# Kernel tuning notes

Hardware: AMD Instinct MI355X
Metric: run time of the kernel (lower is better)

## Reference

```python
import jax, jax.numpy as jnp
import numpy as np

S, B, IN = 8, 8192, 2      # obs seq_len, batch, input_size
E, H, OUT, PRED = 256, 1024, 2, 12  # embed, rnn_size, output_size, pred_len


def setup_inputs() -> dict:
    key = jax.random.key(0)
    ks = jax.random.split(key, 20)
    w = lambda k, shape, fan: (jax.random.normal(k, shape, jnp.float32) / np.sqrt(fan))
    return {
        "obs_traj": jax.random.normal(ks[0], (S, B, IN), jnp.float32),
        # input embedding Linear(IN -> E)
        "W_emb": w(ks[1], (E, IN), IN), "b_emb": jnp.zeros((E,), jnp.float32),
        # LSTM layer 0: input E -> H  (torch gate order i,f,g,o)
        "W_ih0": w(ks[2], (4 * H, E), E), "W_hh0": w(ks[3], (4 * H, H), H),
        "b_ih0": jnp.zeros((4 * H,), jnp.float32), "b_hh0": jnp.zeros((4 * H,), jnp.float32),
        # LSTM layer 1: input H -> H
        "W_ih1": w(ks[4], (4 * H, H), H), "W_hh1": w(ks[5], (4 * H, H), H),
        "b_ih1": jnp.zeros((4 * H,), jnp.float32), "b_hh1": jnp.zeros((4 * H,), jnp.float32),
        # output_seq MLP: H -> 32 -> 16 -> OUT
        "W1": w(ks[6], (32, H), H), "b1": jnp.zeros((32,), jnp.float32),
        "W2": w(ks[7], (16, 32), 32), "b2": jnp.zeros((16,), jnp.float32),
        "W3": w(ks[8], (OUT, 16), 16), "b3": jnp.zeros((OUT,), jnp.float32),
    }


def reference(obs_traj, W_emb, b_emb, W_ih0, W_hh0, b_ih0, b_hh0,
              W_ih1, W_hh1, b_ih1, b_hh1, W1, b1, W2, b2, W3, b3):
    # Dropout layers are identity in eval mode.
    def embed(x):
        return jax.nn.relu(x @ W_emb.T + b_emb)

    def cell(x, h, c, Wih, Whh, bih, bhh):
        g = x @ Wih.T + h @ Whh.T + (bih + bhh)          # [B, 4H]
        i, f, gg, o = jnp.split(g, 4, axis=-1)
        c = jax.nn.sigmoid(f) * c + jax.nn.sigmoid(i) * jnp.tanh(gg)
        h = jax.nn.sigmoid(o) * jnp.tanh(c)
        return h, c

    def lstm_step(hc, x):
        h0, c0, h1, c1 = hc
        h0, c0 = cell(x, h0, c0, W_ih0, W_hh0, b_ih0, b_hh0)
        h1, c1 = cell(h0, h1, c1, W_ih1, W_hh1, b_ih1, b_hh1)
        return (h0, c0, h1, c1), h1

    def mlp(h):
        h = jax.nn.relu(h @ W1.T + b1)
        h = jax.nn.relu(h @ W2.T + b2)
        return h @ W3.T + b3

    z = jnp.zeros((B, H), obs_traj.dtype)
    hc = (z, z, z, z)

    # --- encoding: run LSTM over the observed trajectory ---
    emb_obs = embed(obs_traj)                             # [S, B, E]
    hc, _ = jax.lax.scan(lambda c, x: lstm_step(c, x), hc, emb_obs)

    curr = obs_traj[-1]                                   # [B, IN]
    curr_emb = embed(curr)

    def dec_step(carry, _):
        hc, curr, curr_emb = carry
        hc, out = lstm_step(hc, curr_emb)                 # out: [B, H]
        nxt = curr + mlp(out)                             # displacement decode
        return (hc, nxt, embed(nxt)), nxt

    _, preds = jax.lax.scan(dec_step, (hc, curr, curr_emb), None, length=PRED)
    return preds                                          # [PRED, B, OUT]
```

## Files before the change

kernel.cpp:

```cpp
#include <hip/hip_runtime.h>
#include <hip/hip_bf16.h>
#include <stdint.h>

typedef __hip_bfloat16 bf16;
typedef __attribute__((ext_vector_type(8))) short bf16x8;
typedef __attribute__((ext_vector_type(4))) float f32x4;
typedef __attribute__((ext_vector_type(8))) unsigned short us8;

#define NB 8192
#define NE 256
#define NH 1024

__device__ __forceinline__ float bf2f(unsigned short u) {
  union { unsigned int i; float f; } x; x.i = ((unsigned int)u) << 16; return x.f;
}
__device__ __forceinline__ float sigm(float x) {
  return __builtin_amdgcn_rcpf(1.f + __expf(-x));
}
__device__ __forceinline__ float tanh_f(float x) {
  return 1.f - 2.f * __builtin_amdgcn_rcpf(1.f + __expf(2.f * x));
}

#define BAR() __builtin_amdgcn_s_barrier()
#define FENCE() asm volatile("" ::: "memory")
#define LGKME() asm volatile("s_waitcnt lgkmcnt(0)" ::: "memory")
#define VMW(N) asm volatile("s_waitcnt vmcnt(" #N ")" ::: "memory")

#define GLDS(G, S)                                                            \
  __builtin_amdgcn_global_load_lds(                                           \
      (const __attribute__((address_space(1))) void*)(G),                     \
      (__attribute__((address_space(3))) void*)(S), 16, 0, 0)

#define MFMA32(MH)                                                            \
  do {                                                                        \
    _Pragma("unroll") for (int i_ = 0; i_ < 4; ++i_)                          \
      _Pragma("unroll") for (int g_ = 0; g_ < 4; ++g_) {                      \
        acc[(MH)*4 + i_][g_] = __builtin_amdgcn_mfma_f32_16x16x32_bf16(       \
            af[i_], bv[g_], acc[(MH)*4 + i_][g_], 0, 0, 0);                   \
        acc[(MH)*4 + i_][g_] = __builtin_amdgcn_mfma_f32_16x16x32_bf16(       \
            af[4 + i_], bv[4 + g_], acc[(MH)*4 + i_][g_], 0, 0, 0);           \
      }                                                                       \
  } while (0)

#define LDA8(BUF, MH)                                                         \
  do {                                                                        \
    const char* Ab_ = (const char*)&As[BUF][0][0];                            \
    _Pragma("unroll") for (int i_ = 0; i_ < 4; ++i_) {                        \
      int ro_ = (wr * 128 + (MH)*64 + i_ * 16 + l15) * 128;                   \
      af[i_]     = *(const bf16x8*)(Ab_ + ro_ + co0);                         \
      af[4 + i_] = *(const bf16x8*)(Ab_ + ro_ + co1);                         \
    }                                                                         \
  } while (0)

#define LDB8(BUF)                                                             \
  do {                                                                        \
    const char* Bb_ = (const char*)&Bs[BUF][0][0];                            \
    _Pragma("unroll") for (int g_ = 0; g_ < 4; ++g_) {                        \
      int ro_ = (g_ * 64 + nc * 16 + l15) * 128;                              \
      bv[g_]     = *(const bf16x8*)(Bb_ + ro_ + co0);                         \
      bv[4 + g_] = *(const bf16x8*)(Bb_ + ro_ + co1);                         \
    }                                                                         \
  } while (0)

struct CellP {
  const bf16* X; const bf16* Hin;
  const bf16* Wih; const bf16* Whh;
  const float* bias; float* Cst; bf16* Hout;
  int ldx, Kx, Kh, czero;
};

__global__ __launch_bounds__(512, 2) void k_cell(CellP PA, CellP PB, int nA)
{
  __shared__ bf16 As[2][256][64];
  __shared__ bf16 Bs[2][256][64];

  const CellP p = (blockIdx.x < (unsigned)nA) ? PA : PB;
  const int bid = (blockIdx.x < (unsigned)nA) ? blockIdx.x : (blockIdx.x - nA);

  const int tid = threadIdx.x;
  const int l = tid & 63;
  const int l15 = l & 15;
  const int wv = tid >> 6;
  const int wr = wv >> 2;
  const int nc = wv & 3;

  const int xcd = bid & 7, j = bid >> 3;
  const int m0 = (xcd * 4 + (j & 3)) * 256;
  const int hc0 = (j >> 2) * 64;

  const int NT = (p.Kx + p.Kh) >> 6;
  const int T = NT >> 1;

  const int rowid = tid >> 3;
  const int ch = (tid & 7) ^ (rowid & 7);
  const int ch8 = ch * 8;
  const int wv8 = wv * 8;

  const int co0 = (((l >> 4) + 0) ^ (l & 7)) * 16;
  const int co1 = (((l >> 4) + 4) ^ (l & 7)) * 16;

  f32x4 acc[8][4];
  f32x4 zero4 = {0.f, 0.f, 0.f, 0.f};
#pragma unroll
  for (int i = 0; i < 8; ++i)
#pragma unroll
    for (int j2 = 0; j2 < 4; ++j2) acc[i][j2] = zero4;

  auto stage_a = [&](int buf, int half, int kt) {
    int kc = kt << 6;
    const bf16* src; int ldi;
    if (kc < p.Kx) { src = p.X + kc; ldi = p.ldx; }
    else           { src = p.Hin + (kc - p.Kx); ldi = NH; }
#pragma unroll
    for (int rnd = 0; rnd < 2; ++rnd) {
      int tr = rnd * 128 + half * 64;
      const bf16* gp = src + (unsigned)((m0 + tr + rowid) * ldi + ch8);
      GLDS(gp, &As[buf][tr + wv8][0]);
    }
  };
  auto stage_b = [&](int buf, int half, int kt) {
    int kc = kt << 6;
    const bf16* src; int ldi;
    if (kc < p.Kx) { src = p.Wih + kc; ldi = p.Kx; }
    else           { src = p.Whh + (kc - p.Kx); ldi = NH; }
#pragma unroll
    for (int rnd = 0; rnd < 2; ++rnd) {
      int gate = rnd * 2 + half;
      const bf16* gp = src + (unsigned)((gate * NH + hc0 + rowid) * ldi + ch8);
      GLDS(gp, &Bs[buf][gate * 64 + wv8][0]);
    }
  };

  stage_a(0, 0, 0);
  stage_a(0, 1, 0);
  stage_b(0, 0, 0);
  stage_b(0, 1, 0);
  stage_a(1, 0, 1);
  VMW(2);
  BAR();

  for (int t = 0; t < T; ++t) {
    const int kt1 = 2 * t + 1;
    const bool last = (t == T - 1);
    bf16x8 af[8], bv[8];

    LDB8(0); LDA8(0, 0);
    stage_a(1, 1, kt1);
    stage_b(1, 0, kt1);
    stage_b(1, 1, kt1);
    FENCE(); BAR();
    MFMA32(0);
    LGKME();
    BAR();

    LDA8(0, 1);
    if (!last) stage_a(0, 0, kt1 + 1);
    FENCE(); BAR();
    MFMA32(1);
    LGKME();
    if (last) { VMW(0); } else { VMW(2); }
    BAR();

    LDB8(1); LDA8(1, 0);
    if (!last) {
      stage_a(0, 1, kt1 + 1);
      stage_b(0, 0, kt1 + 1);
      stage_b(0, 1, kt1 + 1);
    }
    FENCE(); BAR();
    MFMA32(0);
    LGKME();
    BAR();

    LDA8(1, 1);
    if (!last) stage_a(1, 0, kt1 + 2);
    FENCE(); BAR();
    MFMA32(1);
    LGKME();
    if (!last) { VMW(2); }
    BAR();
  }

  const int ecol = hc0 + nc * 16 + l15;
  const float bi = p.bias[ecol];
  const float bff = p.bias[NH + ecol];
  const float bg = p.bias[2 * NH + ecol];
  const float bo = p.bias[3 * NH + ecol];
  const int r0 = m0 + wr * 128 + ((l >> 4) << 2);
#pragma unroll
  for (int m = 0; m < 8; ++m) {
#pragma unroll
    for (int r = 0; r < 4; ++r) {
      int row = r0 + m * 16 + r;
      unsigned idx = (unsigned)(row * NH) + ecol;
      float gi = sigm(acc[m][0][r] + bi);
      float gf = sigm(acc[m][1][r] + bff);
      float gg = tanh_f(acc[m][2][r] + bg);
      float go = sigm(acc[m][3][r] + bo);
      float cold = p.czero ? 0.f : p.Cst[idx];
      float cn = gf * cold + gi * gg;
      p.Cst[idx] = cn;
      p.Hout[idx] = __float2bfloat16(go * tanh_f(cn));
    }
  }
}

__global__ __launch_bounds__(256) void k_mlp(
    const bf16* __restrict__ h1, const bf16* __restrict__ W1b, const float* __restrict__ b1,
    const float* __restrict__ W2, const float* __restrict__ b2,
    const float* __restrict__ W3, const float* __restrict__ b3,
    const float* __restrict__ cin, float* __restrict__ cout,
    float* __restrict__ preds, const float* __restrict__ Wemb,
    const float* __restrict__ bemb, bf16* __restrict__ embout)
{
  const int l = threadIdx.x & 63;
  const int row = blockIdx.x * 4 + (threadIdx.x >> 6);

  const us8* hp = (const us8*)(h1 + (size_t)row * NH + l * 16);
  us8 hv0 = hp[0], hv1 = hp[1];
  float h[16];
#pragma unroll
  for (int j = 0; j < 8; ++j) { h[j] = bf2f(hv0[j]); h[8 + j] = bf2f(hv1[j]); }

  float y1[32];
#pragma unroll
  for (int j = 0; j < 32; ++j) {
    const us8* wp = (const us8*)(W1b + (size_t)j * NH + l * 16);
    us8 w0 = wp[0], w1 = wp[1];
    float d = 0.f;
#pragma unroll
    for (int k = 0; k < 8; ++k) {
      d = fmaf(h[k], bf2f(w0[k]), d);
      d = fmaf(h[8 + k], bf2f(w1[k]), d);
    }
#pragma unroll
    for (int off2 = 32; off2 > 0; off2 >>= 1) d += __shfl_xor(d, off2);
    y1[j] = fmaxf(d + b1[j], 0.f);
  }

  float y2[16];
#pragma unroll
  for (int m = 0; m < 16; ++m) {
    float s = b2[m];
#pragma unroll
    for (int j = 0; j < 32; ++j) s = fmaf(W2[m * 32 + j], y1[j], s);
    y2[m] = fmaxf(s, 0.f);
  }
  float o0 = b3[0], o1 = b3[1];
#pragma unroll
  for (int k = 0; k < 16; ++k) {
    o0 = fmaf(W3[k], y2[k], o0);
    o1 = fmaf(W3[16 + k], y2[k], o1);
  }
  float n0 = cin[row * 2] + o0;
  float n1 = cin[row * 2 + 1] + o1;
  if (l == 0) {
    preds[row * 2] = n0; preds[row * 2 + 1] = n1;
    cout[row * 2] = n0;  cout[row * 2 + 1] = n1;
  }
#pragma unroll
  for (int q = 0; q < 4; ++q) {
    int e = l + q * 64;
    float v = fmaf(n0, Wemb[e * 2], fmaf(n1, Wemb[e * 2 + 1], bemb[e]));
    embout[(size_t)row * NE + e] = __float2bfloat16(fmaxf(v, 0.f));
  }
}

__global__ void k_embed(const float* __restrict__ x, const float* __restrict__ W,
                        const float* __restrict__ b, bf16* __restrict__ out) {
  const int l = threadIdx.x & 63;
  const int row = (blockIdx.x * 256 + threadIdx.x) >> 6;
  float x0 = x[row * 2], x1 = x[row * 2 + 1];
#pragma unroll
  for (int q = 0; q < 4; ++q) {
    int e = l + q * 64;
    float v = fmaf(x0, W[e * 2], fmaf(x1, W[e * 2 + 1], b[e]));
    out[(size_t)row * NE + e] = __float2bfloat16(fmaxf(v, 0.f));
  }
}

__global__ void k_f2b(const float* __restrict__ in, bf16* __restrict__ out, int n) {
  int i = (blockIdx.x * 256 + threadIdx.x) * 4;
  if (i >= n) return;
  float4 v = *(const float4*)(in + i);
  out[i] = __float2bfloat16(v.x);
  out[i + 1] = __float2bfloat16(v.y);
  out[i + 2] = __float2bfloat16(v.z);
  out[i + 3] = __float2bfloat16(v.w);
}

__global__ void k_badd(const float* __restrict__ a, const float* __restrict__ b,
                       float* __restrict__ o, int n) {
  int i = blockIdx.x * 256 + threadIdx.x;
  if (i < n) o[i] = a[i] + b[i];
}

extern "C" void kernel_launch(void* const* d_in, const int* in_sizes, int n_in,
                              void* d_out, int out_size, void* d_ws, size_t ws_size,
                              hipStream_t stream) {
  const float* obs   = (const float*)d_in[0];
  const float* Wemb  = (const float*)d_in[1];
  const float* bemb  = (const float*)d_in[2];
  const float* Wih0f = (const float*)d_in[3];
  const float* Whh0f = (const float*)d_in[4];
  const float* bih0  = (const float*)d_in[5];
  const float* bhh0  = (const float*)d_in[6];
  const float* Wih1f = (const float*)d_in[7];
  const float* Whh1f = (const float*)d_in[8];
  const float* bih1  = (const float*)d_in[9];
  const float* bhh1  = (const float*)d_in[10];
  const float* W1f   = (const float*)d_in[11];
  const float* b1m   = (const float*)d_in[12];
  const float* W2    = (const float*)d_in[13];
  const float* b2    = (const float*)d_in[14];
  const float* W3    = (const float*)d_in[15];
  const float* b3    = (const float*)d_in[16];

  char* ws = (char*)d_ws;
  size_t off = 0;
  auto alloc = [&](size_t bytes) -> void* {
    void* p = ws + off;
    off += (bytes + 255) & ~(size_t)255;
    return p;
  };
  bf16* wih0 = (bf16*)alloc((size_t)4096 * 256 * 2);
  bf16* whh0 = (bf16*)alloc((size_t)4096 * 1024 * 2);
  bf16* wih1 = (bf16*)alloc((size_t)4096 * 1024 * 2);
  bf16* whh1 = (bf16*)alloc((size_t)4096 * 1024 * 2);
  bf16* w1b  = (bf16*)alloc((size_t)32 * 1024 * 2);
  float* b0c = (float*)alloc((size_t)4096 * 4);
  float* b1c = (float*)alloc((size_t)4096 * 4);
  bf16* emb  = (bf16*)alloc((size_t)8 * NB * NE * 2);
  bf16* h0a  = (bf16*)alloc((size_t)NB * NH * 2);
  bf16* h0b  = (bf16*)alloc((size_t)NB * NH * 2);
  bf16* h1a  = (bf16*)alloc((size_t)NB * NH * 2);
  bf16* h1b  = (bf16*)alloc((size_t)NB * NH * 2);
  float* c0  = (float*)alloc((size_t)NB * NH * 4);
  float* c1  = (float*)alloc((size_t)NB * NH * 4);
  float* curr = (float*)alloc((size_t)NB * 2 * 4);
  bf16* cemb = (bf16*)alloc((size_t)NB * NE * 2);

  k_f2b<<<1024, 256, 0, stream>>>(Wih0f, wih0, 4096 * 256);
  k_f2b<<<4096, 256, 0, stream>>>(Whh0f, whh0, 4096 * 1024);
  k_f2b<<<4096, 256, 0, stream>>>(Wih1f, wih1, 4096 * 1024);
  k_f2b<<<4096, 256, 0, stream>>>(Whh1f, whh1, 4096 * 1024);
  k_f2b<<<32, 256, 0, stream>>>(W1f, w1b, 32 * 1024);
  k_badd<<<16, 256, 0, stream>>>(bih0, bhh0, b0c, 4096);
  k_badd<<<16, 256, 0, stream>>>(bih1, bhh1, b1c, 4096);
  k_embed<<<(8 * NB) / 4, 256, 0, stream>>>(obs, Wemb, bemb, emb);

  bf16* h0buf[2] = {h0a, h0b};
  bf16* h1buf[2] = {h1a, h1b};
  float* preds = (float*)d_out;

  auto mk = [&](const bf16* X, int ldx, int Kx, const bf16* Hin, int Kh,
                const bf16* Wih, const bf16* Whh, const float* bb, float* C,
                bf16* Ho, int cz) {
    CellP q;
    q.X = X; q.Hin = Hin; q.Wih = Wih; q.Whh = Whh;
    q.bias = bb; q.Cst = C; q.Hout = Ho;
    q.ldx = ldx; q.Kx = Kx; q.Kh = Kh; q.czero = cz;
    return q;
  };

  {
    CellP p0 = mk(emb, NE, NE, h0buf[1], 0, wih0, whh0, b0c, c0, h0buf[0], 1);
    k_cell<<<512, 512, 0, stream>>>(p0, p0, 512);
  }
  for (int t = 0; t < 8; ++t) {
    int cu = t & 1, pv = cu ^ 1;
    int kh1 = (t == 0) ? 0 : NH;
    CellP pl1 = mk(h0buf[cu], NH, NH, h1buf[pv], kh1,
                   wih1, whh1, b1c, c1, h1buf[cu], t == 0);
    const bf16* xnext = (t + 1 < 8) ? emb + (size_t)(t + 1) * NB * NE
                                    : emb + (size_t)7 * NB * NE;
    CellP pl0 = mk(xnext, NE, NE, h0buf[cu], NH,
                   wih0, whh0, b0c, c0, h0buf[pv], 0);
    k_cell<<<1024, 512, 0, stream>>>(pl1, pl0, 512);
  }
  for (int t = 8; t < 20; ++t) {
    int cu = t & 1, pv = cu ^ 1;
    if (t > 8) {
      CellP pl0 = mk(cemb, NE, NE, h0buf[pv], NH,
                     wih0, whh0, b0c, c0, h0buf[cu], 0);
      k_cell<<<512, 512, 0, stream>>>(pl0, pl0, 512);
    }
    CellP pl1 = mk(h0buf[cu], NH, NH, h1buf[pv], NH,
                   wih1, whh1, b1c, c1, h1buf[cu], 0);
    k_cell<<<512, 512, 0, stream>>>(pl1, pl1, 512);
    int pI = t - 8;
    const float* cin = (pI == 0) ? (obs + (size_t)7 * NB * 2) : curr;
    k_mlp<<<NB / 4, 256, 0, stream>>>(h1buf[cu], w1b, b1m, W2, b2, W3, b3,
                                      cin, curr, preds + (size_t)pI * NB * 2,
                                      Wemb, bemb, cemb);
  }
}
```

Before: 4.545 ms.

## Load A operand directly from global into registers, stage only B in LDS

Removes the LDS staging of the activation (A) tile and has each wave read its A fragments straight from global memory into registers. The weight (B) tile is now staged through registers with ordinary vector loads and swizzled LDS writes instead of async global-to-LDS loads. The K loop is split into an input section and a hidden-state section. This halves LDS use and traffic, but A loads now hit global/L2 directly with exposed latency and redundant reads across the waves that share rows.

```diff
diff --git a/kernel.cpp b/kernel.cpp
--- a/kernel.cpp
+++ b/kernel.cpp
@@ -24,12 +24,6 @@
 #define BAR() __builtin_amdgcn_s_barrier()
 #define FENCE() asm volatile("" ::: "memory")
 #define LGKME() asm volatile("s_waitcnt lgkmcnt(0)" ::: "memory")
-#define VMW(N) asm volatile("s_waitcnt vmcnt(" #N ")" ::: "memory")
-
-#define GLDS(G, S)                                                            \
-  __builtin_amdgcn_global_load_lds(                                           \
-      (const __attribute__((address_space(1))) void*)(G),                     \
-      (__attribute__((address_space(3))) void*)(S), 16, 0, 0)
 
 #define MFMA32(MH)                                                            \
   do {                                                                        \
@@ -42,19 +36,18 @@
       }                                                                       \
   } while (0)
 
-#define LDA8(BUF, MH)                                                         \
+#define LDAG(MH, KLOC)                                                        \
   do {                                                                        \
-    const char* Ab_ = (const char*)&As[BUF][0][0];                            \
+    const bf16* ab_ = asec + (KLOC);                                          \
     _Pragma("unroll") for (int i_ = 0; i_ < 4; ++i_) {                        \
-      int ro_ = (wr * 128 + (MH)*64 + i_ * 16 + l15) * 128;                   \
-      af[i_]     = *(const bf16x8*)(Ab_ + ro_ + co0);                         \
-      af[4 + i_] = *(const bf16x8*)(Ab_ + ro_ + co1);                         \
+      af[i_]     = *(const bf16x8*)(ab_ + oa[MH][i_]);                        \
+      af[4 + i_] = *(const bf16x8*)(ab_ + oa[MH][i_] + 32);                   \
     }                                                                         \
   } while (0)
 
 #define LDB8(BUF)                                                             \
   do {                                                                        \
-    const char* Bb_ = (const char*)&Bs[BUF][0][0];                            \
+    const char* Bb_ = Barena + (BUF)*32768;                                   \
     _Pragma("unroll") for (int g_ = 0; g_ < 4; ++g_) {                        \
       int ro_ = (g_ * 64 + nc * 16 + l15) * 128;                              \
       bv[g_]     = *(const bf16x8*)(Bb_ + ro_ + co0);                         \
@@ -71,8 +64,8 @@
 
 __global__ __launch_bounds__(512, 2) void k_cell(CellP PA, CellP PB, int nA)
 {
-  __shared__ bf16 As[2][256][64];
   __shared__ bf16 Bs[2][256][64];
+  char* Barena = (char*)&Bs[0][0][0];
 
   const CellP p = (blockIdx.x < (unsigned)nA) ? PA : PB;
   const int bid = (blockIdx.x < (unsigned)nA) ? blockIdx.x : (blockIdx.x - nA);
@@ -88,17 +81,40 @@
   const int m0 = (xcd * 4 + (j & 3)) * 256;
   const int hc0 = (j >> 2) * 64;
 
-  const int NT = (p.Kx + p.Kh) >> 6;
-  const int T = NT >> 1;
-
-  const int rowid = tid >> 3;
-  const int ch = (tid & 7) ^ (rowid & 7);
-  const int ch8 = ch * 8;
-  const int wv8 = wv * 8;
+  const int NTt = (p.Kx + p.Kh) >> 6;
+  const int TX = p.Kx >> 7;
+  const int TH = p.Kh >> 7;
 
   const int co0 = (((l >> 4) + 0) ^ (l & 7)) * 16;
   const int co1 = (((l >> 4) + 4) ^ (l & 7)) * 16;
 
+  const int row_t = tid >> 3;
+  const int cg = tid & 7;
+  int wadr[4];
+#pragma unroll
+  for (int w = 0; w < 4; ++w) {
+    int row = w * 64 + row_t;
+    wadr[w] = row * 128 + ((cg ^ (row & 7)) << 4);
+  }
+
+  auto bloadg = [&](int kt, f32x4* br) {
+    int kc = kt << 6;
+    const bf16* src; int ldb;
+    if (kc < p.Kx) { src = p.Wih + kc; ldb = p.Kx; }
+    else           { src = p.Whh + (kc - p.Kx); ldb = NH; }
+#pragma unroll
+    for (int w = 0; w < 4; ++w) {
+      int row = w * 64 + row_t;
+      int grow = (row >> 6) * NH + hc0 + (row & 63);
+      br[w] = *(const f32x4*)(src + (unsigned)(grow * ldb + cg * 8));
+    }
+  };
+  auto bwrite = [&](int buf, const f32x4* br) {
+#pragma unroll
+    for (int w = 0; w < 4; ++w)
+      *(f32x4*)(Barena + buf * 32768 + wadr[w]) = br[w];
+  };
+
   f32x4 acc[8][4];
   f32x4 zero4 = {0.f, 0.f, 0.f, 0.f};
 #pragma unroll
@@ -106,80 +122,64 @@
 #pragma unroll
     for (int j2 = 0; j2 < 4; ++j2) acc[i][j2] = zero4;
 
-  auto stage_a = [&](int buf, int half, int kt) {
-    int kc = kt << 6;
-    const bf16* src; int ldi;
-    if (kc < p.Kx) { src = p.X + kc; ldi = p.ldx; }
-    else           { src = p.Hin + (kc - p.Kx); ldi = NH; }
-#pragma unroll
-    for (int rnd = 0; rnd < 2; ++rnd) {
-      int tr = rnd * 128 + half * 64;
-      const bf16* gp = src + (unsigned)((m0 + tr + rowid) * ldi + ch8);
-      GLDS(gp, &As[buf][tr + wv8][0]);
-    }
-  };
-  auto stage_b = [&](int buf, int half, int kt) {
-    int kc = kt << 6;
-    const bf16* src; int ldi;
-    if (kc < p.Kx) { src = p.Wih + kc; ldi = p.Kx; }
-    else           { src = p.Whh + (kc - p.Kx); ldi = NH; }
-#pragma unroll
-    for (int rnd = 0; rnd < 2; ++rnd) {
-      int gate = rnd * 2 + half;
-      const bf16* gp = src + (unsigned)((gate * NH + hc0 + rowid) * ldi + ch8);
-      GLDS(gp, &Bs[buf][gate * 64 + wv8][0]);
-    }
-  };
-
-  stage_a(0, 0, 0);
-  stage_a(0, 1, 0);
-  stage_b(0, 0, 0);
-  stage_b(0, 1, 0);
-  stage_a(1, 0, 1);
-  VMW(2);
+  {
+    f32x4 br[4];
+    bloadg(0, br);
+    bwrite(0, br);
+  }
+  LGKME();
   BAR();
 
-  for (int t = 0; t < T; ++t) {
-    const int kt1 = 2 * t + 1;
-    const bool last = (t == T - 1);
+  auto run_section = [&](const bf16* asec, int ald, int koff, int t0, int tcnt) {
+    if (tcnt == 0) return;
+    unsigned oa[2][4];
+#pragma unroll
+    for (int mh_ = 0; mh_ < 2; ++mh_)
+#pragma unroll
+      for (int i_ = 0; i_ < 4; ++i_)
+        oa[mh_][i_] = (unsigned)((m0 + wr * 128 + mh_ * 64 + i_ * 16 + l15) * ald +
+                                 ((l >> 4) << 3));
     bf16x8 af[8], bv[8];
-
-    LDB8(0); LDA8(0, 0);
-    stage_a(1, 1, kt1);
-    stage_b(1, 0, kt1);
-    stage_b(1, 1, kt1);
-    FENCE(); BAR();
-    MFMA32(0);
-    LGKME();
-    BAR();
-
-    LDA8(0, 1);
-    if (!last) stage_a(0, 0, kt1 + 1);
-    FENCE(); BAR();
-    MFMA32(1);
-    LGKME();
-    if (last) { VMW(0); } else { VMW(2); }
-    BAR();
-
-    LDB8(1); LDA8(1, 0);
-    if (!last) {
-      stage_a(0, 1, kt1 + 1);
-      stage_b(0, 0, kt1 + 1);
-      stage_b(0, 1, kt1 + 1);
-    }
-    FENCE(); BAR();
-    MFMA32(0);
-    LGKME();
-    BAR();
-
-    LDA8(1, 1);
-    if (!last) stage_a(1, 0, kt1 + 2);
-    FENCE(); BAR();
-    MFMA32(1);
-    LGKME();
-    if (!last) { VMW(2); }
-    BAR();
-  }
+    for (int t = t0; t < t0 + tcnt; ++t) {
+      const int kt0 = 2 * t;
+      const int kloc0 = (kt0 << 6) - koff;
+      const bool more = (kt0 + 2 < NTt);
+      f32x4 br[4];
+
+      bloadg(kt0 + 1, br);
+      LDB8(0);
+      LDAG(0, kloc0);
+      FENCE(); BAR();
+      MFMA32(0);
+      LGKME();
+      BAR();
+
+      bwrite(1, br);
+      LDAG(1, kloc0);
+      FENCE(); BAR();
+      MFMA32(1);
+      LGKME();
+      BAR();
+
+      if (more) bloadg(kt0 + 2, br);
+      LDB8(1);
+      LDAG(0, kloc0 + 64);
+      FENCE(); BAR();
+      MFMA32(0);
+      LGKME();
+      BAR();
+
+      if (more) bwrite(0, br);
+      LDAG(1, kloc0 + 64);
+      FENCE(); BAR();
+      MFMA32(1);
+      LGKME();
+      BAR();
+    }
+  };
+
+  run_section(p.X, p.ldx, 0, 0, TX);
+  run_section(p.Hin, NH, p.Kx, TX, TH);
 
   const int ecol = hc0 + nc * 16 + l15;
   const float bi = p.bias[ecol];
```

After: 11.18 ms. +146.0%, slower.
